# Optimization experiments

Hardware: AMD Instinct MI355X
Metric: run time of the kernel (lower is better)

## Reference

```python
import jax, jax.numpy as jnp
import numpy as np

G = 128          # voxel grid extent per axis
B = G + 2        # key base, allows coords in [-1, G] after +1 shift
N_PTS = 100000
C_IN = 32
C_OUT = 32


def _key(c):
    # c: [..., 3] int32 voxel coords in [-1, G]; unique linear key per voxel
    return ((c[..., 0] + 1) * B + (c[..., 1] + 1)) * B + (c[..., 2] + 1)


def setup_inputs() -> dict:
    key = jax.random.key(0)
    k1, k2, k3 = jax.random.split(key, 3)
    positions = jax.random.randint(k1, (N_PTS, 3), 0, G, dtype=jnp.int32)
    features = jax.random.normal(k2, (N_PTS, C_IN), dtype=jnp.float32)
    # per-offset filter matrices, [K^3, Cin, Cout], fan-in style init
    weight = jax.random.normal(k3, (27, C_IN, C_OUT), dtype=jnp.float32) * (1.0 / np.sqrt(27 * C_IN))
    return {"features": features, "positions": positions, "weight": weight}


def reference(features, positions, weight):
    # Submanifold sparse conv: output at the same sparse positions as input.
    # For each of the 27 kernel offsets, hash-lookup the neighbor voxel,
    # gather its feature (or 0 if absent), matmul with the per-offset filter,
    # accumulate. use_bias=False, normalize=False, voxel_size=1.0, offset=0.
    n = features.shape[0]
    keys = _key(positions)                      # [N]
    order = jnp.argsort(keys)
    sk = keys[order]                            # sorted keys (hash table)

    ax = jnp.arange(-1, 2, dtype=jnp.int32)
    off = jnp.stack(jnp.meshgrid(ax, ax, ax, indexing="ij"), axis=-1).reshape(27, 3)

    qk = _key(positions[None, :, :] + off[:, None, :])          # [27, N]
    pos_idx = jnp.clip(jnp.searchsorted(sk, qk), 0, n - 1)      # [27, N]
    match = sk[pos_idx] == qk                                   # neighbor exists?
    gidx = order[pos_idx]                                       # original index of neighbor

    gf = jnp.where(match[..., None], features[gidx], 0.0)       # [27, N, Cin] gather
    out = jnp.einsum("onc,ocd->nd", gf, weight)                 # scatter-accumulate via reduce over o
    return out
```

## Files before the change

### kernel.cpp

```cpp
#include <hip/hip_runtime.h>


#define GRID_B 130
#define GRID_CELLS 2197000
#define BM_WORDS 68704
#define C 32
#define NTHR 256
#define PTS 32
#define CAP 14
#define ROWS_CAP 112

__global__ void build_grid_kernel(const int* __restrict__ pos,
                                  int* __restrict__ grid,
                                  unsigned int* __restrict__ bm, int n) {
    int i = blockIdx.x * blockDim.x + threadIdx.x;
    if (i >= n) return;
    int x = pos[3 * i + 0] + 1;
    int y = pos[3 * i + 1] + 1;
    int z = pos[3 * i + 2] + 1;
    int key = (x * GRID_B + y) * GRID_B + z;
    atomicMax(&grid[key], n - i);
    atomicOr(&bm[key >> 5], 1u << (key & 31));
}

__global__ __launch_bounds__(NTHR)
void conv_kernel(const float* __restrict__ feat,
                 const int* __restrict__ pos,
                 const float* __restrict__ w,
                 const int* __restrict__ grid,
                 const unsigned int* __restrict__ bm,
                 float* __restrict__ out, int n) {
    __shared__ int   s_cnt[27];
    __shared__ int   s_seg[27];
    __shared__ int   s_total;
    __shared__ int   s_list[27][CAP];
    __shared__ int   s_rep[PTS];
    __shared__ int   s_jidx[ROWS_CAP];
    __shared__ int   s_pos[PTS * 3];
    __shared__ __align__(16) float s_rows[ROWS_CAP][C];
    __shared__ __align__(16) float s_acc[PTS][C];

    const int tid = threadIdx.x;
    const int pt_base = blockIdx.x * PTS;

    if (tid < 27) s_cnt[tid] = 0;
    if (tid < PTS * 3) {
        int g = pt_base * 3 + tid;
        if (g < n * 3) s_pos[tid] = pos[g];
    }
    __syncthreads();

    for (int t = tid; t < PTS * 9; t += NTHR) {
        int pl = t / 9;
        int xy = t - pl * 9;
        if (pt_base + pl < n) {
            int dx = xy / 3;
            int dy = xy - dx * 3;
            int x0 = s_pos[pl * 3 + 0] + dx;
            int y0 = s_pos[pl * 3 + 1] + dy;
            int k0 = (x0 * GRID_B + y0) * GRID_B + s_pos[pl * 3 + 2];
            unsigned int w0 = bm[(k0 >> 5)];
            unsigned int w1 = bm[(k0 >> 5) + 1];
            unsigned int bits =
                (unsigned int)((((unsigned long long)w1 << 32) | w0) >> (k0 & 31)) & 7u;
            int obase = xy * 3;
            if (xy == 4) {
                s_rep[pl] = k0 + 1;
                bits &= 5u;
            }
            while (bits) {
                int oz = __ffs(bits) - 1;
                bits &= bits - 1;
                int slot = atomicAdd(&s_cnt[obase + oz], 1);
                if (slot < CAP) s_list[obase + oz][slot] = (pl << 22) | (k0 + oz);
            }
        }
    }
    __syncthreads();

    if (tid < 64) {
        int o = tid;
        int c = (o < 27 && o != 13) ? min(s_cnt[o], CAP) : 0;
        int x = c;
        #pragma unroll
        for (int d = 1; d < 32; d <<= 1) {
            int y = __shfl_up(x, d, 64);
            if (tid >= d) x += y;
        }
        if (o < 27) s_seg[o] = PTS + x - c;
        if (o == 26) s_total = PTS + x;
    }
    __syncthreads();

    for (int t = tid; t < 27 * CAP + PTS; t += NTHR) {
        if (t < 27 * CAP) {
            int o = t / CAP;
            int slot = t - o * CAP;
            if (o != 13 && slot < min(s_cnt[o], CAP)) {
                int f = s_seg[o] + slot;
                if (f < ROWS_CAP)
                    s_jidx[f] = n - grid[s_list[o][slot] & 0x3FFFFF];
            }
        } else {
            int pl = t - 27 * CAP;
            s_jidx[pl] = (pt_base + pl < n) ? (n - grid[s_rep[pl]]) : 0;
        }
    }
    __syncthreads();

    {
        int totc = min(s_total, ROWS_CAP);
        int lane = tid & 63, wv = tid >> 6;
        int nI = (totc + 7) >> 3;
        for (int i = wv; i < nI; i += 4) {
            int f = (i << 3) + (lane >> 3);
            int j = s_jidx[min(f, totc - 1)];
            const float* g = feat + (size_t)j * C + ((lane & 7) << 2);
            __builtin_amdgcn_global_load_lds(
                (const __attribute__((address_space(1))) unsigned int*)g,
                (__attribute__((address_space(3))) unsigned int*)(&s_rows[i << 3][0]),
                16, 0, 0);
        }
    }
    asm volatile("s_waitcnt vmcnt(0)" ::: "memory");
    __syncthreads();

    {
        const int hw8 = tid >> 5;
        const int cout = tid & 31;
        const int cnt13 = min(PTS, n - pt_base);
        float wreg[32];
        #pragma unroll
        for (int c = 0; c < 32; ++c) wreg[c] = w[13 * 1024 + c * 32 + cout];
        for (int e = hw8; e < cnt13; e += 8) {
            const float4* R = (const float4*)(&s_rows[e][0]);
            float acc = 0.0f;
            #pragma unroll
            for (int k = 0; k < 8; ++k) {
                float4 rv = R[k];
                acc = fmaf(rv.x, wreg[4 * k + 0], acc);
                acc = fmaf(rv.y, wreg[4 * k + 1], acc);
                acc = fmaf(rv.z, wreg[4 * k + 2], acc);
                acc = fmaf(rv.w, wreg[4 * k + 3], acc);
            }
            s_acc[e][cout] = acc;
        }
    }
    __syncthreads();

    {
        const int hw8 = tid >> 5;
        const int cout = tid & 31;
        for (int o = hw8; o < 27; o += 8) {
            if (o == 13) continue;
            int cnt = min(s_cnt[o], CAP);
            if (cnt == 0) continue;
            int seg = s_seg[o];
            float wreg[32];
            #pragma unroll
            for (int c = 0; c < 32; ++c) wreg[c] = w[o * 1024 + c * 32 + cout];
            for (int e = 0; e < cnt; ++e) {
                int f = seg + e;
                if (f >= ROWS_CAP) break;
                int pl = ((unsigned int)s_list[o][e]) >> 22;
                const float4* R = (const float4*)(&s_rows[f][0]);
                float acc = 0.0f;
                #pragma unroll
                for (int k = 0; k < 8; ++k) {
                    float4 rv = R[k];
                    acc = fmaf(rv.x, wreg[4 * k + 0], acc);
                    acc = fmaf(rv.y, wreg[4 * k + 1], acc);
                    acc = fmaf(rv.z, wreg[4 * k + 2], acc);
                    acc = fmaf(rv.w, wreg[4 * k + 3], acc);
                }
                atomicAdd(&s_acc[pl][cout], acc);
            }
        }
    }
    __syncthreads();

    {
        const int base = pt_base * C;
        const int lim = n * C - base;
        for (int u = tid; u < PTS * C && u < lim; u += NTHR)
            out[base + u] = s_acc[u >> 5][u & 31];
    }
}

extern "C" void kernel_launch(void* const* d_in, const int* in_sizes, int n_in,
                              void* d_out, int out_size, void* d_ws, size_t ws_size,
                              hipStream_t stream) {
    const float* features = (const float*)d_in[0];
    const int*   positions = (const int*)d_in[1];
    const float* weight = (const float*)d_in[2];
    float* out = (float*)d_out;
    const int n = in_sizes[0] / C;

    int* grid = (int*)d_ws;
    unsigned int* bm = (unsigned int*)(grid + GRID_CELLS);
    hipMemsetAsync(d_ws, 0, (size_t)(GRID_CELLS + BM_WORDS) * sizeof(int), stream);

    build_grid_kernel<<<(n + 255) / 256, 256, 0, stream>>>(positions, grid, bm, n);

    conv_kernel<<<(n + PTS - 1) / PTS, NTHR, 0, stream>>>(features, positions, weight,
                                                          grid, bm, out, n);
}
```

Baseline: 120.5 us.

## Replace dense voxel grid with bitmap rank compaction to avoid large memset

Drops the dense 2.2M-entry index grid and its memset. Occupied voxels are instead ranked with a popcount prefix scan over the occupancy bitmap, and the point index is stored in a compact array of size n. This cuts the memset and scattered-atomic footprint, but adds two scan kernels, an extra rank-building pass and more dependent loads per neighbor lookup in the conv kernel.

New measurement: 127.0 us. 1.05x slower.

```diff
diff --git a/kernel.cpp b/kernel.cpp
--- a/kernel.cpp
+++ b/kernel.cpp
@@ -2,33 +2,91 @@
 
 
 #define GRID_B 130
-#define GRID_CELLS 2197000
-#define BM_WORDS 68704
+#define BMW 68864
+#define NCHUNK 269
 #define C 32
 #define NTHR 256
 #define PTS 32
 #define CAP 14
 #define ROWS_CAP 112
 
-__global__ void build_grid_kernel(const int* __restrict__ pos,
-                                  int* __restrict__ grid,
-                                  unsigned int* __restrict__ bm, int n) {
+__global__ void build_bm_kernel(const int* __restrict__ pos,
+                                unsigned int* __restrict__ bm, int n) {
     int i = blockIdx.x * blockDim.x + threadIdx.x;
     if (i >= n) return;
     int x = pos[3 * i + 0] + 1;
     int y = pos[3 * i + 1] + 1;
     int z = pos[3 * i + 2] + 1;
     int key = (x * GRID_B + y) * GRID_B + z;
-    atomicMax(&grid[key], n - i);
     atomicOr(&bm[key >> 5], 1u << (key & 31));
+}
+
+__global__ void scan1_kernel(const unsigned int* __restrict__ bm,
+                             int* __restrict__ wpref, int* __restrict__ boff) {
+    __shared__ int sc[256];
+    const int t = threadIdx.x;
+    const int wd = blockIdx.x * 256 + t;
+    int c = __popc(bm[wd]);
+    sc[t] = c;
+    __syncthreads();
+    #pragma unroll
+    for (int d = 1; d < 256; d <<= 1) {
+        int v = (t >= d) ? sc[t - d] : 0;
+        __syncthreads();
+        sc[t] += v;
+        __syncthreads();
+    }
+    wpref[wd] = sc[t] - c;
+    if (t == 255) boff[blockIdx.x] = sc[255];
+}
+
+__global__ void scan2_kernel(int* __restrict__ boff) {
+    __shared__ int sc[512];
+    const int t = threadIdx.x;
+    int v = (t < NCHUNK) ? boff[t] : 0;
+    sc[t] = v;
+    __syncthreads();
+    #pragma unroll
+    for (int d = 1; d < 512; d <<= 1) {
+        int x = (t >= d) ? sc[t - d] : 0;
+        __syncthreads();
+        sc[t] += x;
+        __syncthreads();
+    }
+    if (t < NCHUNK) boff[t] = sc[t] - v;
+}
+
+__global__ void build_rank_kernel(const int* __restrict__ pos,
+                                  const unsigned int* __restrict__ bm,
+                                  const int* __restrict__ wpref,
+                                  const int* __restrict__ boff,
+                                  int* __restrict__ rank, int n) {
+    int i = blockIdx.x * blockDim.x + threadIdx.x;
+    if (i >= n) return;
+    int x = pos[3 * i + 0] + 1;
+    int y = pos[3 * i + 1] + 1;
+    int z = pos[3 * i + 2] + 1;
+    int key = (x * GRID_B + y) * GRID_B + z;
+    int wd = key >> 5, b = key & 31;
+    int r = boff[wd >> 8] + wpref[wd] + __popc(bm[wd] & ((1u << b) - 1u));
+    atomicMax(&rank[r], n - i);
+}
+
+__device__ __forceinline__ int rank_of(const unsigned int* __restrict__ bm,
+                                       const int* __restrict__ wpref,
+                                       const int* __restrict__ boff, int key) {
+    int wd = key >> 5, b = key & 31;
+    return boff[wd >> 8] + wpref[wd] + __popc(bm[wd] & ((1u << b) - 1u));
 }
 
 __global__ __launch_bounds__(NTHR)
 void conv_kernel(const float* __restrict__ feat,
                  const int* __restrict__ pos,
                  const float* __restrict__ w,
-                 const int* __restrict__ grid,
                  const unsigned int* __restrict__ bm,
+                 const int* __restrict__ wpref,
+                 const int* __restrict__ boff,
+                 const int* __restrict__ rank,
                  float* __restrict__ out, int n) {
     __shared__ int   s_cnt[27];
     __shared__ int   s_seg[27];
@@ -98,12 +156,15 @@
             int slot = t - o * CAP;
             if (o != 13 && slot < min(s_cnt[o], CAP)) {
                 int f = s_seg[o] + slot;
-                if (f < ROWS_CAP)
-                    s_jidx[f] = n - grid[s_list[o][slot] & 0x3FFFFF];
+                if (f < ROWS_CAP) {
+                    int key = s_list[o][slot] & 0x3FFFFF;
+                    s_jidx[f] = n - rank[rank_of(bm, wpref, boff, key)];
+                }
             }
         } else {
             int pl = t - 27 * CAP;
-            s_jidx[pl] = (pt_base + pl < n) ? (n - grid[s_rep[pl]]) : 0;
+            s_jidx[pl] = (pt_base + pl < n)
+                       ? (n - rank[rank_of(bm, wpref, boff, s_rep[pl])]) : 0;
         }
     }
     __syncthreads();
@@ -196,12 +257,19 @@
     float* out = (float*)d_out;
     const int n = in_sizes[0] / C;
 
-    int* grid = (int*)d_ws;
-    unsigned int* bm = (unsigned int*)(grid + GRID_CELLS);
-    hipMemsetAsync(d_ws, 0, (size_t)(GRID_CELLS + BM_WORDS) * sizeof(int), stream);
-
-    build_grid_kernel<<<(n + 255) / 256, 256, 0, stream>>>(positions, grid, bm, n);
-
+    unsigned int* bm = (unsigned int*)d_ws;
+    int* rank  = (int*)d_ws + BMW;
+    int* wpref = (int*)d_ws + BMW + n;
+    int* boff  = (int*)d_ws + BMW + n + BMW;
+
+    hipMemsetAsync(d_ws, 0, (size_t)(BMW + n) * sizeof(int), stream);
+
+    build_bm_kernel<<<(n + 255) / 256, 256, 0, stream>>>(positions, bm, n);
+    scan1_kernel<<<NCHUNK, 256, 0, stream>>>(bm, wpref, boff);
+    scan2_kernel<<<1, 512, 0, stream>>>(boff);
+    build_rank_kernel<<<(n + 255) / 256, 256, 0, stream>>>(positions, bm, wpref,
+                                                           boff, rank, n);
     conv_kernel<<<(n + PTS - 1) / PTS, NTHR, 0, stream>>>(features, positions, weight,
-                                                          grid, bm, out, n);
-}
+                                                          bm, wpref, boff, rank,
+                                                          out, n);
+}
```
